# Kernel optimization log

Measured on AMD Instinct MI355X. Metric: run time of the kernel, lower is better.

## Reference

```python
import jax, jax.numpy as jnp
import numpy as np

N, T, D = 2, 2048, 1024
H, HW = 16, 64  # num_heads, head_width
NEG = -1e9


def setup_inputs() -> dict:
    key = jax.random.key(0)
    kx, kq, kk, kv = jax.random.split(key, 4)
    x = jax.random.normal(kx, (N, T, D), dtype=jnp.float32)
    # additive causal mask: 0 on/below diagonal, large negative above
    causal = jnp.triu(jnp.ones((T, T), dtype=jnp.float32), k=1) * NEG
    mask = causal[None, None]  # [1,1,T,T]
    s = 1.0 / np.sqrt(D)
    Wq = jax.random.normal(kq, (D, D), dtype=jnp.float32) * s
    Wk = jax.random.normal(kk, (D, D), dtype=jnp.float32) * s
    Wv = jax.random.normal(kv, (D, D), dtype=jnp.float32) * s
    return {"x": x, "mask": mask, "Wq": Wq, "Wk": Wk, "Wv": Wv}


def _alibi_bias(t):
    # slopes: 2^(-i*8/H) for i = 1..H, shape [H,1,1]
    step = 8.0 / H
    slopes = 2.0 ** (-step * jnp.arange(1, H + 1, dtype=jnp.float32))
    rel = (jnp.arange(t)[None, :] - jnp.arange(t)[:, None]).astype(jnp.float32)  # [t,t], rel[i,j]=j-i
    return slopes[:, None, None] * rel[None]  # [H,t,t]


def reference(x, mask, Wq, Wk, Wv):
    n, t, d = x.shape

    def heads(w):
        # nn.Linear: x @ W^T, then split into heads -> [n,H,t,HW]
        return (x @ w.T).reshape(n, t, H, HW).transpose(0, 2, 1, 3)

    q, k, v = heads(Wq), heads(Wk), heads(Wv)
    att = jnp.einsum("bhqd,bhkd->bhqk", q, k) / np.sqrt(HW)
    att = att + _alibi_bias(t)[None] + mask[:, :, :t, :t]
    att = jax.nn.softmax(att, axis=-1)
    res = jnp.einsum("bhqk,bhkd->bhqd", att, v)
    return res.transpose(0, 2, 1, 3).reshape(n, t, d)
```

## Files before the change

kernel.cpp:

```cpp
#include <hip/hip_runtime.h>
#include <stdint.h>

#define N_B 2
#define T_SEQ 2048
#define D_MODEL 1024
#define N_HEADS 16
#define HEAD_W 64

typedef __attribute__((ext_vector_type(8))) short short8;
typedef __attribute__((ext_vector_type(4))) float f32x4;

#define GLOAD_LDS16(gp, lp)                                                          \
    __builtin_amdgcn_global_load_lds((__attribute__((address_space(1))) void*)(gp),  \
                                     (__attribute__((address_space(3))) void*)(lp),  \
                                     16, 0, 0)

__device__ __forceinline__ unsigned short f2bf(float f) {
    union { float f; uint32_t u; } cv; cv.f = f;
    return (unsigned short)((cv.u + 0x7fffu + ((cv.u >> 16) & 1u)) >> 16);
}

__device__ __forceinline__ uint32_t cvt_pk_bf16(float lo, float hi) {
    uint32_t r;
    asm("v_cvt_pk_bf16_f32 %0, %1, %2" : "=v"(r) : "v"(lo), "v"(hi));
    return r;
}

__device__ __forceinline__ float bf2f(uint32_t us) {
    union { uint32_t u; float f; } cv; cv.u = us << 16; return cv.f;
}

#define LOG2E 1.44269504f

__global__ __launch_bounds__(256) void cvt_fused(const float4* __restrict__ x,
                                                 const float4* __restrict__ wq,
                                                 const float4* __restrict__ wk,
                                                 const float4* __restrict__ wv,
                                                 uint64_t* __restrict__ xb,
                                                 uint64_t* __restrict__ wqb,
                                                 uint64_t* __restrict__ wkb,
                                                 uint64_t* __restrict__ wvb) {
    const int i = blockIdx.x * 256 + threadIdx.x;
    const float4* src; uint64_t* dst; float scale; int off;
    if (i < 1048576)      { src = x;  dst = xb;  scale = 1.f;            off = i; }
    else if (i < 1310720) { src = wq; dst = wqb; scale = 0.125f * LOG2E; off = i - 1048576; }
    else if (i < 1572864) { src = wk; dst = wkb; scale = 1.f;            off = i - 1310720; }
    else                  { src = wv; dst = wvb; scale = 1.f;            off = i - 1572864; }
    float4 v = src[off];
    union { unsigned short us[4]; uint64_t u64; } o;
    o.us[0] = f2bf(v.x * scale);
    o.us[1] = f2bf(v.y * scale);
    o.us[2] = f2bf(v.z * scale);
    o.us[3] = f2bf(v.w * scale);
    dst[off] = o.u64;
}

__global__ __launch_bounds__(256, 4) void qkv_gemm(const unsigned short* __restrict__ A,
                                                   const unsigned short* __restrict__ W0,
                                                   const unsigned short* __restrict__ W1,
                                                   const unsigned short* __restrict__ W2,
                                                   unsigned short* __restrict__ O0,
                                                   unsigned short* __restrict__ O1,
                                                   unsigned short* __restrict__ O2) {
    __shared__ union {
        struct { unsigned short A[128 * 64]; unsigned short W[128 * 64]; } st;
        unsigned short vb[4][64 * 72];
    } sh;
    const int bid0 = blockIdx.x;
    const int bid = (bid0 & 7) * 96 + (bid0 >> 3);
    const int z = bid >> 8;
    const int rem = bid & 255;
    const int m0 = (rem >> 3) * 128;
    const int n0 = (rem & 7) * 128;
    const unsigned short* W = (z == 0) ? W0 : (z == 1) ? W1 : W2;
    const int tid = threadIdx.x;
    const int lane = tid & 63;
    const int ww = tid >> 6;
    const int wr = (ww >> 1) * 64;
    const int wc = (ww & 1) * 64;
    const int g = lane >> 4;
    const int fr = lane & 15;
    const int srow = lane >> 3;
    const int sgr = (lane & 7) ^ srow;

    f32x4 acc[4][4];
#pragma unroll
    for (int i = 0; i < 4; ++i)
#pragma unroll
        for (int j = 0; j < 4; ++j) acc[i][j] = (f32x4){0.f, 0.f, 0.f, 0.f};

    for (int k0 = 0; k0 < D_MODEL; k0 += 64) {
#pragma unroll
        for (int it = 0; it < 4; ++it) {
            const int chunk = ww * 4 + it;
            const int row = chunk * 8 + srow;
            GLOAD_LDS16(A + (size_t)(m0 + row) * D_MODEL + k0 + sgr * 8,
                        (unsigned short*)sh.st.A + chunk * 512);
            GLOAD_LDS16(W + (size_t)(n0 + row) * D_MODEL + k0 + sgr * 8,
                        (unsigned short*)sh.st.W + chunk * 512);
        }
        __syncthreads();
#pragma unroll
        for (int kb = 0; kb < 2; ++kb) {
            short8 af[4], bf[4];
#pragma unroll
            for (int mi = 0; mi < 4; ++mi) {
                const int row = wr + mi * 16 + fr;
                af[mi] = *(const short8*)(sh.st.A + row * 64 +
                                          (((kb * 4 + g) ^ (fr & 7)) * 8));
            }
#pragma unroll
            for (int ni = 0; ni < 4; ++ni) {
                const int row = wc + ni * 16 + fr;
                bf[ni] = *(const short8*)(sh.st.W + row * 64 +
                                          (((kb * 4 + g) ^ (fr & 7)) * 8));
            }
#pragma unroll
            for (int mi = 0; mi < 4; ++mi)
#pragma unroll
                for (int ni = 0; ni < 4; ++ni)
                    acc[mi][ni] = __builtin_amdgcn_mfma_f32_16x16x32_bf16(af[mi], bf[ni],
                                                                          acc[mi][ni], 0, 0, 0);
        }
        __syncthreads();
    }

    const int ro = g * 4;
    if (z < 2) {
        unsigned short* outp = (z == 0) ? O0 : O1;
#pragma unroll
        for (int mi = 0; mi < 4; ++mi)
#pragma unroll
            for (int ni = 0; ni < 4; ++ni)
#pragma unroll
                for (int r = 0; r < 4; ++r)
                    sh.vb[ww][(mi * 16 + ro + r) * 72 + ni * 16 + fr] = f2bf(acc[mi][ni][r]);
        const int hh = (n0 + wc) >> 6;
        const int colb = (lane & 7) * 8;
#pragma unroll
        for (int rep = 0; rep < 8; ++rep) {
            const int rl = rep * 8 + (lane >> 3);
            const int m = m0 + wr + rl;
            const int b = m >> 11, t = m & (T_SEQ - 1);
            short8 vv = *(const short8*)(&sh.vb[ww][rl * 72 + colb]);
            *(short8*)(outp + ((size_t)(b * N_HEADS + hh) * T_SEQ + t) * HEAD_W + colb) = vv;
        }
    } else {
#pragma unroll
        for (int mi = 0; mi < 4; ++mi)
#pragma unroll
            for (int ni = 0; ni < 4; ++ni)
#pragma unroll
                for (int r = 0; r < 4; ++r)
                    sh.vb[ww][(ni * 16 + fr) * 72 + mi * 16 + ro + r] = f2bf(acc[mi][ni][r]);
#pragma unroll
        for (int rep = 0; rep < 8; ++rep) {
            const int nl = rep * 8 + (lane >> 3);
            const int n = n0 + wc + nl;
            const int h = n >> 6, wd = n & (HEAD_W - 1);
            const int m = m0 + wr + (lane & 7) * 8;
            const int b = m >> 11, t = m & (T_SEQ - 1);
            short8 vv = *(const short8*)(&sh.vb[ww][nl * 72 + (lane & 7) * 8]);
            *(short8*)(O2 + ((size_t)(b * N_HEADS + h) * HEAD_W + wd) * T_SEQ + t) = vv;
        }
    }
}

__global__ __launch_bounds__(256, 5) void attn_fwd(const unsigned short* __restrict__ Qb,
                                                   const unsigned short* __restrict__ Kb,
                                                   const unsigned short* __restrict__ Vtb,
                                                   float* __restrict__ outp,
                                                   unsigned short* __restrict__ opart,
                                                   float* __restrict__ lpart) {
    __shared__ unsigned short Kl[2][64 * 64];
    __shared__ unsigned short Vl[2][64 * 64];

    const int bid = blockIdx.x;
    int ib, ck;
    if (bid < 1024)      { ck = 0; ib = bid; }
    else if (bid < 1536) { ck = 1; ib = bid - 1024; }
    else                 { ck = 2; ib = bid - 1536; }
    const int qi = 31 - (ib >> 5);
    const int b = (ib >> 4) & 1;
    const int h = ((ib & 15) + 5 * (ib >> 8)) & 15;
    const int q0 = qi * 64;
    const int tid = threadIdx.x, lane = tid & 63, w = tid >> 6;
    const int qw = q0 + w * 16;
    const float slope2 = exp2f(-0.5f * (float)(h + 1)) * LOG2E;

    const float tlf = ((float)q0 - 63.0f - 40.0f / slope2) * 0.015625f;
    const int t_lo = (tlf > 0.0f) ? (int)ceilf(tlf) : 0;

    const bool deep = (qi >= 16);
    const bool single = !deep || (t_lo > qi - 16);
    int t_start, t_end;
    if (ck == 0) {
        t_start = qi;
        t_end = single ? t_lo : (qi - 15);
    } else if (ck == 1) {
        t_start = qi - 16;
        t_end = (t_lo > qi - 23) ? t_lo : (qi - 23);
        if (t_start < t_end) return;
    } else {
        t_start = qi - 24;
        t_end = t_lo;
        if (t_start < t_end) return;
    }
    const int slot = (((qi - 16) << 5) | (h << 1) | b) + (ck << 9);

    const unsigned short* Qp = Qb + (size_t)(b * N_HEADS + h) * T_SEQ * HEAD_W;
    const unsigned short* Kp = Kb + (size_t)(b * N_HEADS + h) * T_SEQ * HEAD_W;
    const unsigned short* Vp = Vtb + (size_t)(b * N_HEADS + h) * HEAD_W * T_SEQ;

    const int g = lane >> 4, c = lane & 15;
    const int srow = lane >> 3;
    const int sgr = (lane & 7) ^ srow;
    const bool ghi = (g >= 2);

#define STAGE_KV(buf, k0_)                                                               \
    {                                                                                    \
        _Pragma("unroll")                                                                \
        for (int it = 0; it < 2; ++it) {                                                 \
            const int ch = w * 2 + it;                                                   \
            const int row = ch * 8 + srow;                                               \
            GLOAD_LDS16(Kp + (size_t)((k0_) + row) * HEAD_W + sgr * 8,                   \
                        (unsigned short*)Kl[buf] + ch * 512);                            \
            GLOAD_LDS16(Vp + (size_t)row * T_SEQ + (k0_) + sgr * 8,                      \
                        (unsigned short*)Vl[buf] + ch * 512);                            \
        }                                                                                \
    }

    short8 qf[2];
#pragma unroll
    for (int kb = 0; kb < 2; ++kb)
        qf[kb] = *(const short8*)(Qp + (size_t)(qw + c) * HEAD_W + kb * 32 + g * 8);

    float K16[4][4];
#pragma unroll
    for (int ct = 0; ct < 4; ++ct)
#pragma unroll
        for (int r = 0; r < 4; ++r)
            K16[ct][r] = slope2 * (float)(ct * 16 + g * 4 + r - qw - c) - 30.0f;

    union { uint32_t u[4]; short8 s8; } one_u;
#pragma unroll
    for (int i = 0; i < 4; ++i) one_u.u[i] = 0x3F803F80u;
    const short8 ones8 = one_u.s8;

    f32x4 o[4];
#pragma unroll
    for (int i = 0; i < 4; ++i) o[i] = (f32x4){0.f, 0.f, 0.f, 0.f};
    f32x4 lac = (f32x4){0.f, 0.f, 0.f, 0.f};

    STAGE_KV(t_start & 1, t_start * 64);
    __syncthreads();

    for (int t = t_start; t >= t_end; --t) {
        const int k0 = t * 64;
        if (t > t_end) STAGE_KV((t - 1) & 1, k0 - 64);
        const unsigned short* Kt = Kl[t & 1];
        const unsigned short* Vt = Vl[t & 1];

        const float ut = slope2 * (float)k0;
        f32x4 s[4];
#pragma unroll
        for (int ct = 0; ct < 4; ++ct)
#pragma unroll
            for (int r = 0; r < 4; ++r) s[ct][r] = K16[ct][r] + ut;
        __builtin_amdgcn_s_setprio(1);
#pragma unroll
        for (int ct = 0; ct < 4; ++ct)
#pragma unroll
            for (int kb = 0; kb < 2; ++kb) {
                const short8 kf = *(const short8*)(Kt + (ct * 16 + c) * 64 +
                                                   (((kb * 4 + g) ^ (c & 7)) * 8));
                s[ct] = __builtin_amdgcn_mfma_f32_16x16x32_bf16(kf, qf[kb], s[ct], 0, 0, 0);
            }
        __builtin_amdgcn_s_setprio(0);

        if (t == qi) {
            const int ri = w * 16 + c - g * 4;
#pragma unroll
            for (int ct = 0; ct < 4; ++ct)
#pragma unroll
                for (int r = 0; r < 4; ++r)
                    s[ct][r] = (ct * 16 + r > ri) ? -1e30f : s[ct][r];
        }

        uint32_t pk[4][2];
#pragma unroll
        for (int ct = 0; ct < 4; ++ct) {
            float p[4];
#pragma unroll
            for (int r = 0; r < 4; ++r)
                p[r] = exp2f(s[ct][r]);
            pk[ct][0] = cvt_pk_bf16(p[0], p[1]);
            pk[ct][1] = cvt_pk_bf16(p[2], p[3]);
        }

#pragma unroll
        for (int kb = 0; kb < 2; ++kb) {
            uint32_t pu[4];
#pragma unroll
            for (int v = 0; v < 2; ++v) {
                const uint32_t s0v = ghi ? pk[2 * kb + 1][v] : pk[2 * kb][v];
                const uint32_t s1v = ghi ? pk[2 * kb][v]     : pk[2 * kb + 1][v];
                const uint32_t x16 = __shfl_xor(s0v, 16);
                const uint32_t x32 = __shfl_xor(s1v, 32);
                const uint32_t x48 = __shfl_xor(s1v, 48);
                pu[v]     = (g == 0) ? s0v : (g == 1) ? x48 : (g == 2) ? x32 : x16;
                pu[2 + v] = (g == 0) ? x16 : (g == 1) ? x32 : (g == 2) ? x48 : s0v;
            }
            union { uint32_t u[4]; short8 s8; } pa;
            pa.u[0] = pu[0]; pa.u[1] = pu[1]; pa.u[2] = pu[2]; pa.u[3] = pu[3];
            __builtin_amdgcn_s_setprio(1);
#pragma unroll
            for (int db = 0; db < 4; ++db) {
                const short8 vf = *(const short8*)(Vt + (db * 16 + c) * 64 +
                                                   (((kb * 4 + g) ^ (c & 7)) * 8));
                o[db] = __builtin_amdgcn_mfma_f32_16x16x32_bf16(pa.s8, vf, o[db], 0, 0, 0);
            }
            lac = __builtin_amdgcn_mfma_f32_16x16x32_bf16(pa.s8, ones8, lac, 0, 0, 0);
            __builtin_amdgcn_s_setprio(0);
        }
        __syncthreads();
    }

    if (single) {
        float linv[4];
#pragma unroll
        for (int r = 0; r < 4; ++r) linv[r] = 1.0f / lac[r];
#pragma unroll
        for (int db = 0; db < 4; ++db)
#pragma unroll
            for (int r = 0; r < 4; ++r)
                outp[((size_t)b * T_SEQ + qw + g * 4 + r) * D_MODEL + h * HEAD_W + db * 16 + c] =
                    o[db][r] * linv[r];
    } else {
        uint64_t* op64 = (uint64_t*)(opart + (size_t)slot * 4096 + tid * 16);
#pragma unroll
        for (int db = 0; db < 4; ++db) {
            const uint32_t lo = cvt_pk_bf16(o[db][0], o[db][1]);
            const uint32_t hi = cvt_pk_bf16(o[db][2], o[db][3]);
            op64[db] = (uint64_t)lo | ((uint64_t)hi << 32);
        }
        if (c == 0)
            *(f32x4*)(lpart + slot * 64 + w * 16 + g * 4) = lac;
    }
#undef STAGE_KV
}

__global__ __launch_bounds__(256) void attn_reduce(const unsigned short* __restrict__ opart,
                                                   const float* __restrict__ lpart,
                                                   float* __restrict__ outp) {
    const int slot = blockIdx.x;
    const int qi = 16 + (slot >> 5);
    const int h = (slot & 31) >> 1;
    const int b = slot & 1;
    const float slope2 = exp2f(-0.5f * (float)(h + 1)) * LOG2E;
    const int q0 = qi * 64;
    const float tlf = ((float)q0 - 63.0f - 40.0f / slope2) * 0.015625f;
    const int t_lo = (tlf > 0.0f) ? (int)ceilf(tlf) : 0;
    if (t_lo > qi - 16) return;
    const bool has1b = (t_lo <= qi - 24);

    const int tid = threadIdx.x, lane = tid & 63, w = tid >> 6;
    const int g = lane >> 4, c = lane & 15;
    const int rowb = w * 16 + g * 4;

    const uint64_t* p0 = (const uint64_t*)(opart + (size_t)slot * 4096 + tid * 16);
    const uint64_t* p1 = (const uint64_t*)(opart + (size_t)(slot + 512) * 4096 + tid * 16);
    const uint64_t* p2 = (const uint64_t*)(opart + (size_t)(slot + 1024) * 4096 + tid * 16);

    float linv[4];
#pragma unroll
    for (int r = 0; r < 4; ++r) {
        float lsum = lpart[slot * 64 + rowb + r] + lpart[(slot + 512) * 64 + rowb + r];
        if (has1b) lsum += lpart[(slot + 1024) * 64 + rowb + r];
        linv[r] = 1.0f / lsum;
    }

#pragma unroll
    for (int db = 0; db < 4; ++db) {
        const uint64_t a = p0[db];
        const uint64_t bb = p1[db];
        const uint64_t cc = has1b ? p2[db] : 0ull;
#pragma unroll
        for (int r = 0; r < 4; ++r) {
            float s = bf2f((uint32_t)((a >> (16 * r)) & 0xFFFFu)) +
                      bf2f((uint32_t)((bb >> (16 * r)) & 0xFFFFu));
            if (has1b) s += bf2f((uint32_t)((cc >> (16 * r)) & 0xFFFFu));
            outp[((size_t)b * T_SEQ + q0 + rowb + r) * D_MODEL + h * HEAD_W + db * 16 + c] =
                s * linv[r];
        }
    }
}

extern "C" void kernel_launch(void* const* d_in, const int* in_sizes, int n_in,
                              void* d_out, int out_size, void* d_ws, size_t ws_size,
                              hipStream_t stream) {
    const float* x  = (const float*)d_in[0];
    const float* Wq = (const float*)d_in[2];
    const float* Wk = (const float*)d_in[3];
    const float* Wv = (const float*)d_in[4];
    float* out = (float*)d_out;

    uint8_t* ws = (uint8_t*)d_ws;
    unsigned short* xb  = (unsigned short*)(ws);
    unsigned short* wqb = (unsigned short*)(ws + 8388608);
    unsigned short* wkb = (unsigned short*)(ws + 10485760);
    unsigned short* wvb = (unsigned short*)(ws + 12582912);
    unsigned short* Qb  = (unsigned short*)(ws + 14680064);
    unsigned short* Kb  = (unsigned short*)(ws + 23068672);
    unsigned short* Vtb = (unsigned short*)(ws + 31457280);
    unsigned short* opart = (unsigned short*)(ws);
    float*          lpart = (float*)(ws + 12582912);

    cvt_fused<<<7168, 256, 0, stream>>>((const float4*)x, (const float4*)Wq,
                                        (const float4*)Wk, (const float4*)Wv,
                                        (uint64_t*)xb, (uint64_t*)wqb,
                                        (uint64_t*)wkb, (uint64_t*)wvb);

    qkv_gemm<<<768, 256, 0, stream>>>(xb, wqb, wkb, wvb, Qb, Kb, Vtb);

    attn_fwd<<<2048, 256, 0, stream>>>(Qb, Kb, Vtb, out, opart, lpart);
    attn_reduce<<<512, 256, 0, stream>>>(opart, lpart, out);
}
```

Before: 77.81 us.

## Double query tile per block to 128 rows, reusing K/V fragments across two tiles

Each attention block now processes 128 query rows, two 16-row tiles per wave, instead of 64. Every K and V fragment read from LDS feeds two MFMAs, which halves the K/V staging and LDS traffic per query and halves the grid. Chunk splitting, masking thresholds and partial-slot indexing in the reduce kernel are reworked to match. The cost is more accumulator registers, so the occupancy hint drops from 5 to 4 blocks, plus coarser causal load balancing with fewer blocks.

```diff
diff --git a/kernel.cpp b/kernel.cpp
--- a/kernel.cpp
+++ b/kernel.cpp
@@ -166,7 +166,7 @@
     }
 }
 
-__global__ __launch_bounds__(256, 5) void attn_fwd(const unsigned short* __restrict__ Qb,
+__global__ __launch_bounds__(256, 4) void attn_fwd(const unsigned short* __restrict__ Qb,
                                                    const unsigned short* __restrict__ Kb,
                                                    const unsigned short* __restrict__ Vtb,
                                                    float* __restrict__ outp,
@@ -177,36 +177,36 @@
 
     const int bid = blockIdx.x;
     int ib, ck;
-    if (bid < 1024)      { ck = 0; ib = bid; }
-    else if (bid < 1536) { ck = 1; ib = bid - 1024; }
-    else                 { ck = 2; ib = bid - 1536; }
-    const int qi = 31 - (ib >> 5);
+    if (bid < 512)      { ck = 0; ib = bid; }
+    else if (bid < 768) { ck = 1; ib = bid - 512; }
+    else                { ck = 2; ib = bid - 768; }
+    const int qi = 15 - (ib >> 5);
     const int b = (ib >> 4) & 1;
     const int h = ((ib & 15) + 5 * (ib >> 8)) & 15;
-    const int q0 = qi * 64;
+    const int q0 = qi * 128;
     const int tid = threadIdx.x, lane = tid & 63, w = tid >> 6;
-    const int qw = q0 + w * 16;
+    const int qw = q0 + w * 32;
     const float slope2 = exp2f(-0.5f * (float)(h + 1)) * LOG2E;
 
     const float tlf = ((float)q0 - 63.0f - 40.0f / slope2) * 0.015625f;
     const int t_lo = (tlf > 0.0f) ? (int)ceilf(tlf) : 0;
-
-    const bool deep = (qi >= 16);
-    const bool single = !deep || (t_lo > qi - 16);
+    const int t_hi = 2 * qi + 1;
+
+    const bool single = (t_lo > t_hi - 16);
     int t_start, t_end;
     if (ck == 0) {
-        t_start = qi;
-        t_end = single ? t_lo : (qi - 15);
+        t_start = t_hi;
+        t_end = single ? t_lo : (t_hi - 15);
     } else if (ck == 1) {
-        t_start = qi - 16;
-        t_end = (t_lo > qi - 23) ? t_lo : (qi - 23);
+        t_start = t_hi - 16;
+        t_end = (t_lo > t_hi - 23) ? t_lo : (t_hi - 23);
         if (t_start < t_end) return;
     } else {
-        t_start = qi - 24;
+        t_start = t_hi - 24;
         t_end = t_lo;
         if (t_start < t_end) return;
     }
-    const int slot = (((qi - 16) << 5) | (h << 1) | b) + (ck << 9);
+    const int slot = (((qi - 8) << 5) | (h << 1) | b) + (ck << 8);
 
     const unsigned short* Qp = Qb + (size_t)(b * N_HEADS + h) * T_SEQ * HEAD_W;
     const unsigned short* Kp = Kb + (size_t)(b * N_HEADS + h) * T_SEQ * HEAD_W;
@@ -230,27 +230,36 @@
         }                                                                                \
     }
 
-    short8 qf[2];
-#pragma unroll
-    for (int kb = 0; kb < 2; ++kb)
-        qf[kb] = *(const short8*)(Qp + (size_t)(qw + c) * HEAD_W + kb * 32 + g * 8);
-
-    float K16[4][4];
-#pragma unroll
-    for (int ct = 0; ct < 4; ++ct)
-#pragma unroll
-        for (int r = 0; r < 4; ++r)
-            K16[ct][r] = slope2 * (float)(ct * 16 + g * 4 + r - qw - c) - 30.0f;
+    short8 qf[2][2];
+#pragma unroll
+    for (int qt = 0; qt < 2; ++qt)
+#pragma unroll
+        for (int kb = 0; kb < 2; ++kb)
+            qf[qt][kb] = *(const short8*)(Qp + (size_t)(qw + qt * 16 + c) * HEAD_W +
+                                          kb * 32 + g * 8);
+
+    float ctp[4], rp4[4];
+#pragma unroll
+    for (int ct = 0; ct < 4; ++ct) ctp[ct] = slope2 * (float)(ct * 16);
+#pragma unroll
+    for (int r = 0; r < 4; ++r)
+        rp4[r] = slope2 * (float)(g * 4 + r - qw - c) - 30.0f;
+    const float sl16 = slope2 * 16.0f;
+    const int maskthr = 2 * qi + (w >> 1);
 
     union { uint32_t u[4]; short8 s8; } one_u;
 #pragma unroll
     for (int i = 0; i < 4; ++i) one_u.u[i] = 0x3F803F80u;
     const short8 ones8 = one_u.s8;
 
-    f32x4 o[4];
-#pragma unroll
-    for (int i = 0; i < 4; ++i) o[i] = (f32x4){0.f, 0.f, 0.f, 0.f};
-    f32x4 lac = (f32x4){0.f, 0.f, 0.f, 0.f};
+    f32x4 o[2][4];
+    f32x4 lac[2];
+#pragma unroll
+    for (int qt = 0; qt < 2; ++qt) {
+        lac[qt] = (f32x4){0.f, 0.f, 0.f, 0.f};
+#pragma unroll
+        for (int i = 0; i < 4; ++i) o[qt][i] = (f32x4){0.f, 0.f, 0.f, 0.f};
+    }
 
     STAGE_KV(t_start & 1, t_start * 64);
     __syncthreads();
@@ -260,13 +269,17 @@
         if (t > t_end) STAGE_KV((t - 1) & 1, k0 - 64);
         const unsigned short* Kt = Kl[t & 1];
         const unsigned short* Vt = Vl[t & 1];
-
         const float ut = slope2 * (float)k0;
-        f32x4 s[4];
-#pragma unroll
-        for (int ct = 0; ct < 4; ++ct)
-#pragma unroll
-            for (int r = 0; r < 4; ++r) s[ct][r] = K16[ct][r] + ut;
+
+        f32x4 s[2][4];
+#pragma unroll
+        for (int qt = 0; qt < 2; ++qt) {
+            const float utq = ut - sl16 * (float)qt;
+#pragma unroll
+            for (int ct = 0; ct < 4; ++ct)
+#pragma unroll
+                for (int r = 0; r < 4; ++r) s[qt][ct][r] = ctp[ct] + (rp4[r] + utq);
+        }
         __builtin_amdgcn_s_setprio(1);
 #pragma unroll
         for (int ct = 0; ct < 4; ++ct)
@@ -274,78 +287,100 @@
             for (int kb = 0; kb < 2; ++kb) {
                 const short8 kf = *(const short8*)(Kt + (ct * 16 + c) * 64 +
                                                    (((kb * 4 + g) ^ (c & 7)) * 8));
-                s[ct] = __builtin_amdgcn_mfma_f32_16x16x32_bf16(kf, qf[kb], s[ct], 0, 0, 0);
+                s[0][ct] = __builtin_amdgcn_mfma_f32_16x16x32_bf16(kf, qf[0][kb],
+                                                                   s[0][ct], 0, 0, 0);
+                s[1][ct] = __builtin_amdgcn_mfma_f32_16x16x32_bf16(kf, qf[1][kb],
+                                                                   s[1][ct], 0, 0, 0);
             }
         __builtin_amdgcn_s_setprio(0);
 
-        if (t == qi) {
-            const int ri = w * 16 + c - g * 4;
-#pragma unroll
-            for (int ct = 0; ct < 4; ++ct)
-#pragma unroll
-                for (int r = 0; r < 4; ++r)
-                    s[ct][r] = (ct * 16 + r > ri) ? -1e30f : s[ct][r];
-        }
-
-        uint32_t pk[4][2];
-#pragma unroll
-        for (int ct = 0; ct < 4; ++ct) {
-            float p[4];
-#pragma unroll
-            for (int r = 0; r < 4; ++r)
-                p[r] = exp2f(s[ct][r]);
-            pk[ct][0] = cvt_pk_bf16(p[0], p[1]);
-            pk[ct][1] = cvt_pk_bf16(p[2], p[3]);
-        }
-
-#pragma unroll
-        for (int kb = 0; kb < 2; ++kb) {
-            uint32_t pu[4];
-#pragma unroll
-            for (int v = 0; v < 2; ++v) {
-                const uint32_t s0v = ghi ? pk[2 * kb + 1][v] : pk[2 * kb][v];
-                const uint32_t s1v = ghi ? pk[2 * kb][v]     : pk[2 * kb + 1][v];
-                const uint32_t x16 = __shfl_xor(s0v, 16);
-                const uint32_t x32 = __shfl_xor(s1v, 32);
-                const uint32_t x48 = __shfl_xor(s1v, 48);
-                pu[v]     = (g == 0) ? s0v : (g == 1) ? x48 : (g == 2) ? x32 : x16;
-                pu[2 + v] = (g == 0) ? x16 : (g == 1) ? x32 : (g == 2) ? x48 : s0v;
-            }
-            union { uint32_t u[4]; short8 s8; } pa;
-            pa.u[0] = pu[0]; pa.u[1] = pu[1]; pa.u[2] = pu[2]; pa.u[3] = pu[3];
-            __builtin_amdgcn_s_setprio(1);
+        union { uint32_t u[4]; short8 s8; } pa[2][2];
+#pragma unroll
+        for (int qt = 0; qt < 2; ++qt) {
+            if (t >= maskthr) {
+                const int ri = qw + qt * 16 + c - k0 - g * 4;
+#pragma unroll
+                for (int ct = 0; ct < 4; ++ct)
+#pragma unroll
+                    for (int r = 0; r < 4; ++r)
+                        s[qt][ct][r] = (ct * 16 + r > ri) ? -1e30f : s[qt][ct][r];
+            }
+            uint32_t pk[4][2];
+#pragma unroll
+            for (int ct = 0; ct < 4; ++ct) {
+                float p[4];
+#pragma unroll
+                for (int r = 0; r < 4; ++r) p[r] = exp2f(s[qt][ct][r]);
+                pk[ct][0] = cvt_pk_bf16(p[0], p[1]);
+                pk[ct][1] = cvt_pk_bf16(p[2], p[3]);
+            }
+#pragma unroll
+            for (int kb = 0; kb < 2; ++kb)
+#pragma unroll
+                for (int v = 0; v < 2; ++v) {
+                    const uint32_t s0v = ghi ? pk[2 * kb + 1][v] : pk[2 * kb][v];
+                    const uint32_t s1v = ghi ? pk[2 * kb][v]     : pk[2 * kb + 1][v];
+                    const uint32_t x16 = __shfl_xor(s0v, 16);
+                    const uint32_t x32 = __shfl_xor(s1v, 32);
+                    const uint32_t x48 = __shfl_xor(s1v, 48);
+                    pa[qt][kb].u[v]     = (g == 0) ? s0v : (g == 1) ? x48 :
+                                          (g == 2) ? x32 : x16;
+                    pa[qt][kb].u[2 + v] = (g == 0) ? x16 : (g == 1) ? x32 :
+                                          (g == 2) ? x48 : s0v;
+                }
+        }
+
+        __builtin_amdgcn_s_setprio(1);
+#pragma unroll
+        for (int kb = 0; kb < 2; ++kb)
 #pragma unroll
             for (int db = 0; db < 4; ++db) {
                 const short8 vf = *(const short8*)(Vt + (db * 16 + c) * 64 +
                                                    (((kb * 4 + g) ^ (c & 7)) * 8));
-                o[db] = __builtin_amdgcn_mfma_f32_16x16x32_bf16(pa.s8, vf, o[db], 0, 0, 0);
-            }
-            lac = __builtin_amdgcn_mfma_f32_16x16x32_bf16(pa.s8, ones8, lac, 0, 0, 0);
-            __builtin_amdgcn_s_setprio(0);
-        }
+                o[0][db] = __builtin_amdgcn_mfma_f32_16x16x32_bf16(pa[0][kb].s8, vf,
+                                                                   o[0][db], 0, 0, 0);
+                o[1][db] = __builtin_amdgcn_mfma_f32_16x16x32_bf16(pa[1][kb].s8, vf,
+                                                                   o[1][db], 0, 0, 0);
+            }
+#pragma unroll
+        for (int kb = 0; kb < 2; ++kb) {
+            lac[0] = __builtin_amdgcn_mfma_f32_16x16x32_bf16(pa[0][kb].s8, ones8,
+                                                             lac[0], 0, 0, 0);
+            lac[1] = __builtin_amdgcn_mfma_f32_16x16x32_bf16(pa[1][kb].s8, ones8,
+                                                             lac[1], 0, 0, 0);
+        }
+        __builtin_amdgcn_s_setprio(0);
         __syncthreads();
     }
 
     if (single) {
-        float linv[4];
-#pragma unroll
-        for (int r = 0; r < 4; ++r) linv[r] = 1.0f / lac[r];
-#pragma unroll
-        for (int db = 0; db < 4; ++db)
-#pragma unroll
-            for (int r = 0; r < 4; ++r)
-                outp[((size_t)b * T_SEQ + qw + g * 4 + r) * D_MODEL + h * HEAD_W + db * 16 + c] =
-                    o[db][r] * linv[r];
+#pragma unroll
+        for (int qt = 0; qt < 2; ++qt) {
+            float linv[4];
+#pragma unroll
+            for (int r = 0; r < 4; ++r) linv[r] = 1.0f / lac[qt][r];
+#pragma unroll
+            for (int db = 0; db < 4; ++db)
+#pragma unroll
+                for (int r = 0; r < 4; ++r)
+                    outp[((size_t)b * T_SEQ + qw + qt * 16 + g * 4 + r) * D_MODEL +
+                         h * HEAD_W + db * 16 + c] = o[qt][db][r] * linv[r];
+        }
     } else {
-        uint64_t* op64 = (uint64_t*)(opart + (size_t)slot * 4096 + tid * 16);
-#pragma unroll
-        for (int db = 0; db < 4; ++db) {
-            const uint32_t lo = cvt_pk_bf16(o[db][0], o[db][1]);
-            const uint32_t hi = cvt_pk_bf16(o[db][2], o[db][3]);
-            op64[db] = (uint64_t)lo | ((uint64_t)hi << 32);
-        }
-        if (c == 0)
-            *(f32x4*)(lpart + slot * 64 + w * 16 + g * 4) = lac;
+        uint64_t* op64 = (uint64_t*)(opart + (size_t)slot * 8192 + tid * 32);
+#pragma unroll
+        for (int qt = 0; qt < 2; ++qt)
+#pragma unroll
+            for (int db = 0; db < 4; ++db) {
+                const uint32_t lo = cvt_pk_bf16(o[qt][db][0], o[qt][db][1]);
+                const uint32_t hi = cvt_pk_bf16(o[qt][db][2], o[qt][db][3]);
+                op64[qt * 4 + db] = (uint64_t)lo | ((uint64_t)hi << 32);
+            }
+        if (c == 0) {
+#pragma unroll
+            for (int qt = 0; qt < 2; ++qt)
+                *(f32x4*)(lpart + slot * 128 + w * 32 + qt * 16 + g * 4) = lac[qt];
+        }
     }
 #undef STAGE_KV
 }
@@ -353,45 +388,48 @@
 __global__ __launch_bounds__(256) void attn_reduce(const unsigned short* __restrict__ opart,
                                                    const float* __restrict__ lpart,
                                                    float* __restrict__ outp) {
-    const int slot = blockIdx.x;
-    const int qi = 16 + (slot >> 5);
-    const int h = (slot & 31) >> 1;
-    const int b = slot & 1;
+    const int bid = blockIdx.x;
+    const int qi = 8 + (bid >> 5);
+    const int h = (bid >> 1) & 15;
+    const int b = bid & 1;
     const float slope2 = exp2f(-0.5f * (float)(h + 1)) * LOG2E;
-    const int q0 = qi * 64;
+    const int q0 = qi * 128;
     const float tlf = ((float)q0 - 63.0f - 40.0f / slope2) * 0.015625f;
     const int t_lo = (tlf > 0.0f) ? (int)ceilf(tlf) : 0;
-    if (t_lo > qi - 16) return;
-    const bool has1b = (t_lo <= qi - 24);
-
+    if (t_lo > 2 * qi - 15) return;
+    const bool has1b = (t_lo <= 2 * qi - 23);
+
+    const int key = ((qi - 8) << 5) | (h << 1) | b;
     const int tid = threadIdx.x, lane = tid & 63, w = tid >> 6;
     const int g = lane >> 4, c = lane & 15;
-    const int rowb = w * 16 + g * 4;
-
-    const uint64_t* p0 = (const uint64_t*)(opart + (size_t)slot * 4096 + tid * 16);
-    const uint64_t* p1 = (const uint64_t*)(opart + (size_t)(slot + 512) * 4096 + tid * 16);
-    const uint64_t* p2 = (const uint64_t*)(opart + (size_t)(slot + 1024) * 4096 + tid * 16);
-
-    float linv[4];
-#pragma unroll
-    for (int r = 0; r < 4; ++r) {
-        float lsum = lpart[slot * 64 + rowb + r] + lpart[(slot + 512) * 64 + rowb + r];
-        if (has1b) lsum += lpart[(slot + 1024) * 64 + rowb + r];
-        linv[r] = 1.0f / lsum;
-    }
-
-#pragma unroll
-    for (int db = 0; db < 4; ++db) {
-        const uint64_t a = p0[db];
-        const uint64_t bb = p1[db];
-        const uint64_t cc = has1b ? p2[db] : 0ull;
+
+    const uint64_t* p0 = (const uint64_t*)(opart + (size_t)key * 8192 + tid * 32);
+    const uint64_t* p1 = (const uint64_t*)(opart + (size_t)(key + 256) * 8192 + tid * 32);
+    const uint64_t* p2 = (const uint64_t*)(opart + (size_t)(key + 512) * 8192 + tid * 32);
+
+#pragma unroll
+    for (int qt = 0; qt < 2; ++qt) {
+        const int rowb = w * 32 + qt * 16 + g * 4;
+        float linv[4];
 #pragma unroll
         for (int r = 0; r < 4; ++r) {
-            float s = bf2f((uint32_t)((a >> (16 * r)) & 0xFFFFu)) +
-                      bf2f((uint32_t)((bb >> (16 * r)) & 0xFFFFu));
-            if (has1b) s += bf2f((uint32_t)((cc >> (16 * r)) & 0xFFFFu));
-            outp[((size_t)b * T_SEQ + q0 + rowb + r) * D_MODEL + h * HEAD_W + db * 16 + c] =
-                s * linv[r];
+            float lsum = lpart[key * 128 + rowb + r] + lpart[(key + 256) * 128 + rowb + r];
+            if (has1b) lsum += lpart[(key + 512) * 128 + rowb + r];
+            linv[r] = 1.0f / lsum;
+        }
+#pragma unroll
+        for (int db = 0; db < 4; ++db) {
+            const uint64_t a = p0[qt * 4 + db];
+            const uint64_t bb = p1[qt * 4 + db];
+            const uint64_t cc = has1b ? p2[qt * 4 + db] : 0ull;
+#pragma unroll
+            for (int r = 0; r < 4; ++r) {
+                float s = bf2f((uint32_t)((a >> (16 * r)) & 0xFFFFu)) +
+                          bf2f((uint32_t)((bb >> (16 * r)) & 0xFFFFu));
+                if (has1b) s += bf2f((uint32_t)((cc >> (16 * r)) & 0xFFFFu));
+                outp[((size_t)b * T_SEQ + q0 + rowb + r) * D_MODEL + h * HEAD_W +
+                     db * 16 + c] = s * linv[r];
+            }
         }
     }
 }
@@ -423,6 +461,6 @@
 
     qkv_gemm<<<768, 256, 0, stream>>>(xb, wqb, wkb, wvb, Qb, Kb, Vtb);
 
-    attn_fwd<<<2048, 256, 0, stream>>>(Qb, Kb, Vtb, out, opart, lpart);
-    attn_reduce<<<512, 256, 0, stream>>>(opart, lpart, out);
-}
+    attn_fwd<<<1024, 256, 0, stream>>>(Qb, Kb, Vtb, out, opart, lpart);
+    attn_reduce<<<256, 256, 0, stream>>>(opart, lpart, out);
+}
```

New measurement: 99.64 us. 28.1% more time.
